# Kernel optimization log

Measured on AMD Instinct MI355X. Metric: run time of the kernel, lower is better.

The kernel has to match this reference:

```python
import jax, jax.numpy as jnp
import numpy as np

B, C, HD, H, W = 4, 64, 64, 64, 64  # batch, input_dim, hidden_dim, spatial


def conv1x1(x, w, b):
    # x: [B, Cin, H, W], w: [Cout, Cin], b: [Cout]
    return jnp.einsum('oc,bchw->bohw', w, x) + b[None, :, None, None]


def setup_inputs() -> dict:
    key = jax.random.key(0)
    ks = jax.random.split(key, 16)
    sc = lambda cin: 1.0 / np.sqrt(cin)
    d = {
        'h': jax.random.normal(ks[0], (B, C, H, W), jnp.float32),
        'm': jax.random.normal(ks[1], (B, C, H, W), jnp.float32),
        'Wq': jax.random.normal(ks[2], (HD, C), jnp.float32) * sc(C),
        'bq': jnp.zeros((HD,), jnp.float32),
        'Wk': jax.random.normal(ks[3], (HD, C), jnp.float32) * sc(C),
        'bk': jnp.zeros((HD,), jnp.float32),
        'Wk2': jax.random.normal(ks[4], (HD, C), jnp.float32) * sc(C),
        'bk2': jnp.zeros((HD,), jnp.float32),
        'Wv': jax.random.normal(ks[5], (C, C), jnp.float32) * sc(C),
        'bv': jnp.zeros((C,), jnp.float32),
        'Wv2': jax.random.normal(ks[6], (C, C), jnp.float32) * sc(C),
        'bv2': jnp.zeros((C,), jnp.float32),
        'Wz': jax.random.normal(ks[7], (2 * C, 2 * C), jnp.float32) * sc(2 * C),
        'bz': jnp.zeros((2 * C,), jnp.float32),
        'Wm': jax.random.normal(ks[8], (3 * C, 3 * C), jnp.float32) * sc(3 * C),
        'bm': jnp.zeros((3 * C,), jnp.float32),
    }
    return d


def reference(h, m, Wq, bq, Wk, bk, Wk2, bk2, Wv, bv, Wv2, bv2, Wz, bz, Wm, bm):
    b, c, hh, ww = h.shape
    n = hh * ww
    K_h = conv1x1(h, Wk, bk).reshape(b, HD, n)            # [B, HD, N]
    Q_h = conv1x1(h, Wq, bq).reshape(b, HD, n).transpose(0, 2, 1)  # [B, N, HD]
    V_h = conv1x1(h, Wv, bv).reshape(b, c, n)             # [B, C, N]
    K_m = conv1x1(m, Wk2, bk2).reshape(b, HD, n)
    V_m = conv1x1(m, Wv2, bv2).reshape(b, c, n)

    A_h = jax.nn.softmax(jnp.einsum('bnd,bdk->bnk', Q_h, K_h), axis=-1)  # [B, N, N]
    Z_h = jnp.einsum('bnk,bck->bcn', A_h, V_h).reshape(b, c, hh, ww)
    A_m = jax.nn.softmax(jnp.einsum('bnd,bdk->bnk', Q_h, K_m), axis=-1)
    Z_m = jnp.einsum('bnk,bck->bcn', A_m, V_m).reshape(b, c, hh, ww)

    Z = conv1x1(jnp.concatenate([Z_h, Z_m], axis=1), Wz, bz)   # [B, 2C, H, W]
    combined = conv1x1(jnp.concatenate([Z, h], axis=1), Wm, bm)  # [B, 3C, H, W]
    mo, mg, mi = jnp.split(combined, 3, axis=1)
    mi = jax.nn.sigmoid(mi)
    new_m = (1.0 - mi) * m + mi * jnp.tanh(mg)
    new_h = jax.nn.sigmoid(mo) * new_m
    return (new_h, new_m)
```

## Files before the change

kernel.cpp:

```cpp
#include <hip/hip_runtime.h>

#define BN 4
#define NN 4096
#define SPLITK 4
#define KTILE 64
#define LOG2E 1.44269504f
#define MFIX 36.0f

typedef __attribute__((ext_vector_type(8))) __bf16 bf16x8;
typedef __attribute__((ext_vector_type(8))) short s16x8;
typedef __attribute__((ext_vector_type(4))) float f32x4;
typedef unsigned short u16;

__device__ __forceinline__ u16 f2bf(float x) {
  unsigned int u = __builtin_bit_cast(unsigned int, x);
  u = (u + 0x7fffu + ((u >> 16) & 1u)) >> 16;
  return (u16)u;
}
__device__ __forceinline__ u16 f2bfs(float x) {
  __bf16 b = (__bf16)x;
  return __builtin_bit_cast(u16, b);
}

__device__ __forceinline__ float fexp2(float x) {
#if defined(__HIP_DEVICE_COMPILE__) && __has_builtin(__builtin_amdgcn_exp2f)
  return __builtin_amdgcn_exp2f(x);
#else
  return __builtin_exp2f(x);
#endif
}

__device__ __forceinline__ f32x4 mfma32(bf16x8 a, bf16x8 b, f32x4 c) {
#if defined(__HIP_DEVICE_COMPILE__)
  return __builtin_amdgcn_mfma_f32_16x16x32_bf16(a, b, c, 0, 0, 0);
#else
  (void)a; (void)b;
  return c;
#endif
}

__device__ __forceinline__ void gld16(const u16* g, u16* l) {
#if defined(__HIP_DEVICE_COMPILE__)
  __builtin_amdgcn_global_load_lds(
      (const __attribute__((address_space(1))) void*)g,
      (__attribute__((address_space(3))) void*)l, 16, 0, 0);
#else
  (void)g; (void)l;
#endif
}

#if defined(__HIP_DEVICE_COMPILE__)
#define SETPRIO(p) __builtin_amdgcn_s_setprio(p)
#else
#define SETPRIO(p)
#endif

#define PACK16(A, P0, P1)                                                          \
    P0.x = (unsigned)f2bf(A[0]) | ((unsigned)f2bf(A[1]) << 16);                    \
    P0.y = (unsigned)f2bf(A[2]) | ((unsigned)f2bf(A[3]) << 16);                    \
    P0.z = (unsigned)f2bf(A[4]) | ((unsigned)f2bf(A[5]) << 16);                    \
    P0.w = (unsigned)f2bf(A[6]) | ((unsigned)f2bf(A[7]) << 16);                    \
    P1.x = (unsigned)f2bf(A[8]) | ((unsigned)f2bf(A[9]) << 16);                    \
    P1.y = (unsigned)f2bf(A[10]) | ((unsigned)f2bf(A[11]) << 16);                  \
    P1.z = (unsigned)f2bf(A[12]) | ((unsigned)f2bf(A[13]) << 16);                  \
    P1.w = (unsigned)f2bf(A[14]) | ((unsigned)f2bf(A[15]) << 16);

__global__ __launch_bounds__(256) void fuse_w2_kernel(
    const float* __restrict__ Wz, const float* __restrict__ bz,
    const float* __restrict__ Wm, const float* __restrict__ bm,
    u16* __restrict__ Wbig, float* __restrict__ bbig) {
  __shared__ float wrow[128];
  __shared__ float bzs[128];
  int o = blockIdx.x;
  int t = threadIdx.x;
  if (t < 128) { wrow[t] = Wm[o * 192 + t]; bzs[t] = bz[t]; }
  __syncthreads();
  if (t < 128) {
    float s = 0.f;
#pragma unroll 4
    for (int j = 0; j < 128; ++j) s = fmaf(wrow[j], Wz[j * 128 + t], s);
    Wbig[o * 192 + t] = f2bf(s);
  } else if (t < 192) {
    Wbig[o * 192 + t] = f2bf(Wm[o * 192 + t]);
  } else if (t == 192) {
    float s = bm[o];
    for (int j = 0; j < 128; ++j) s = fmaf(wrow[j], bzs[j], s);
    bbig[o] = s;
  }
}

__global__ __launch_bounds__(256) void proj3_kernel(
    const float* __restrict__ h, const float* __restrict__ m,
    const float* __restrict__ Wq, const float* __restrict__ bq,
    const float* __restrict__ Wk, const float* __restrict__ bk,
    const float* __restrict__ Wk2, const float* __restrict__ bk2,
    const float* __restrict__ Wv, const float* __restrict__ bv,
    const float* __restrict__ Wv2, const float* __restrict__ bv2,
    u16* __restrict__ Q, u16* __restrict__ Kh, u16* __restrict__ Km,
    u16* __restrict__ Vh, u16* __restrict__ Vm, u16* __restrict__ hT) {
  __shared__ float xs[64][65];
  __shared__ float Wl[4096];
  int blk = blockIdx.x;
  int ntile = blk & 63, b = (blk >> 6) & 3, pid = blk >> 8;
  int n0 = ntile * 64;
  int t = threadIdx.x, nl = t & 63;
  const float* src = (pid == 2 || pid == 4) ? m : h;
  {
    int c0 = (t >> 6) * 16;
#pragma unroll
    for (int i = 0; i < 16; ++i) {
      int c = c0 + i;
      xs[c][nl] = src[((size_t)(b * 64) + c) * NN + n0 + nl];
    }
  }
  if (pid < 5) {
    const float* W = pid == 0 ? Wq : pid == 1 ? Wk : pid == 2 ? Wk2 : pid == 3 ? Wv : Wv2;
#pragma unroll
    for (int i = 0; i < 16; ++i) Wl[i * 256 + t] = W[i * 256 + t];
  }
  __syncthreads();
  int w = __builtin_amdgcn_readfirstlane(t >> 6);
  size_t nrow = (size_t)b * NN + n0 + nl;
  float acc[16];
  if (pid == 5) {
#pragma unroll
    for (int i = 0; i < 16; ++i) acc[i] = xs[w * 16 + i][nl];
  } else {
    const float* bs = pid == 0 ? bq : pid == 1 ? bk : pid == 2 ? bk2 : pid == 3 ? bv : bv2;
#pragma unroll
    for (int i = 0; i < 16; ++i) acc[i] = bs[w * 16 + i];
    for (int c = 0; c < 64; ++c) {
      float x = xs[c][nl];
#pragma unroll
      for (int i = 0; i < 16; ++i) acc[i] = fmaf(Wl[(w * 16 + i) * 64 + c], x, acc[i]);
    }
    if (pid == 0) {
#pragma unroll
      for (int i = 0; i < 16; ++i) acc[i] *= LOG2E;
    }
  }
  if (pid == 3 || pid == 4) {
    u16* dst = (pid == 3) ? Vh : Vm;
    int key = n0 + nl;
    size_t base = ((size_t)b << 18) + (size_t)(key >> 5) * 2048 + w * 512 +
                  (size_t)((key >> 3) & 3) * 128 + (key & 7);
#pragma unroll
    for (int i = 0; i < 16; ++i) dst[base + i * 8] = f2bf(acc[i]);
  } else {
    u16* dst = pid == 0 ? Q : pid == 1 ? Kh : pid == 2 ? Km : hT;
    uint4 p0, p1;
    PACK16(acc, p0, p1);
    uint4* dp = (uint4*)(dst + nrow * 64 + w * 16);
    dp[0] = p0; dp[1] = p1;
  }
}

__global__ __launch_bounds__(256, 4) void flash11_kernel(
    const u16* __restrict__ Qg, const u16* __restrict__ Khg,
    const u16* __restrict__ Kmg, const u16* __restrict__ Vhg,
    const u16* __restrict__ Vmg, u16* __restrict__ Opart,
    float* __restrict__ Lpart) {
  __shared__ u16 Kl[2][4096];
  __shared__ u16 Vl[2][4096];
  int blk = blockIdx.x;
  int combo = blk & 31, qt = blk >> 5;
  int attn = combo & 1, b = (combo >> 1) & 3, split = combo >> 3;
  const u16* K = (attn ? Kmg : Khg) + (size_t)b * NN * 64;
  const u16* V = (attn ? Vmg : Vhg) + ((size_t)b << 18);
  int t = threadIdx.x, wave = t >> 6, lane = t & 63, col = lane & 15, quad = lane >> 4;
  int row0 = qt * 128 + wave * 32;

  bf16x8 bq[2][2];
#pragma unroll
  for (int g = 0; g < 2; ++g) {
    const u16* qp = Qg + (size_t)b * NN * 64 + (size_t)(row0 + g * 16 + col) * 64 + quad * 8;
    bq[g][0] = *(const bf16x8*)(const void*)qp;
    bq[g][1] = *(const bf16x8*)(const void*)(qp + 32);
  }

  f32x4 O[2][4];
#pragma unroll
  for (int g = 0; g < 2; ++g)
#pragma unroll
    for (int i = 0; i < 4; ++i) O[g][i] = f32x4{0.f, 0.f, 0.f, 0.f};
  f32x4 Lacc[2];
  Lacc[0] = f32x4{0.f, 0.f, 0.f, 0.f};
  Lacc[1] = f32x4{0.f, 0.f, 0.f, 0.f};
  const f32x4 minit = {-MFIX, -MFIX, -MFIX, -MFIX};
  s16x8 onesv;
#pragma unroll
  for (int i = 0; i < 8; ++i) onesv[i] = (short)0x3F80;
  bf16x8 ones8 = __builtin_bit_cast(bf16x8, onesv);
  int sp = split * 8 + b * 2 + attn;

  const int kbase = split * (NN / SPLITK);
  const int TILES = NN / SPLITK / KTILE;

#define STAGE(BUF, K0)                                                           \
  _Pragma("unroll") for (int jj = 0; jj < 2; ++jj) {                             \
    int p = jj * 256 + t;                                                        \
    int krow_ = p >> 3;                                                          \
    int kj_ = (p & 7) ^ (krow_ & 7);                                             \
    int s5_ = krow_ & 31;                                                        \
    int tr_ = (krow_ & 32) | ((s5_ & 12) << 1) | (((s5_ >> 4) & 1) << 2) | (s5_ & 3); \
    gld16(K + (size_t)((K0) + tr_) * 64 + kj_ * 8, &Kl[BUF][p * 8]);             \
    gld16(V + (size_t)(K0) * 64 + p * 8, &Vl[BUF][p * 8]);                       \
  }

  STAGE(0, kbase);

  for (int kt = 0; kt < TILES; ++kt) {
    __syncthreads();
    int cur = kt & 1;
    if (kt + 1 < TILES) { STAGE(cur ^ 1, kbase + (kt + 1) * KTILE); }
    const u16* Kb = &Kl[cur][0];
    const u16* Vb = &Vl[cur][0];
    f32x4 St[4][2];
    SETPRIO(1);
#pragma unroll
    for (int nt = 0; nt < 4; ++nt) {
      int row = nt * 16 + col;
      int ph0 = row * 8 + (quad ^ (col & 7));
      int ph1 = row * 8 + ((4 + quad) ^ (col & 7));
      bf16x8 a0 = *(const bf16x8*)(const void*)(Kb + ph0 * 8);
      bf16x8 a1 = *(const bf16x8*)(const void*)(Kb + ph1 * 8);
#pragma unroll
      for (int g = 0; g < 2; ++g) {
        f32x4 acc = mfma32(a0, bq[g][0], minit);
        acc = mfma32(a1, bq[g][1], acc);
        St[nt][g] = acc;
      }
    }
    SETPRIO(0);
    bf16x8 pa[2][2];
#pragma unroll
    for (int grp = 0; grp < 2; ++grp)
#pragma unroll
      for (int g = 0; g < 2; ++g) {
        s16x8 pf;
#pragma unroll
        for (int r = 0; r < 4; ++r) {
          pf[r] = (short)f2bfs(fexp2(St[2 * grp][g][r]));
          pf[r + 4] = (short)f2bfs(fexp2(St[2 * grp + 1][g][r]));
        }
        bf16x8 p8 = __builtin_bit_cast(bf16x8, pf);
        pa[grp][g] = p8;
        Lacc[g] = mfma32(p8, ones8, Lacc[g]);
      }
    const u16* vbase = Vb + lane * 8;
    SETPRIO(1);
#pragma unroll
    for (int grp = 0; grp < 2; ++grp)
#pragma unroll
      for (int ct = 0; ct < 4; ++ct) {
        bf16x8 vf = *(const bf16x8*)(const void*)(vbase + grp * 2048 + ct * 512);
        O[0][ct] = mfma32(pa[grp][0], vf, O[0][ct]);
        O[1][ct] = mfma32(pa[grp][1], vf, O[1][ct]);
      }
    SETPRIO(0);
  }
#undef STAGE

#pragma unroll
  for (int g = 0; g < 2; ++g) {
#pragma unroll
    for (int ct = 0; ct < 4; ++ct)
#pragma unroll
      for (int r = 0; r < 4; ++r) {
        size_t q = (size_t)row0 + g * 16 + quad * 4 + r;
        Opart[((size_t)sp * NN + q) * 64 + ct * 16 + col] = f2bfs(O[g][ct][r]);
      }
    if (col == 0) {
#pragma unroll
      for (int r = 0; r < 4; ++r)
        Lpart[(size_t)sp * NN + row0 + g * 16 + quad * 4 + r] = Lacc[g][r];
    }
  }
}

__global__ __launch_bounds__(256) void epi3_kernel(
    const u16* __restrict__ Wb, const float* __restrict__ bb,
    const u16* __restrict__ Opart, const float* __restrict__ Lpart,
    const u16* __restrict__ hT, const float* __restrict__ mglob,
    float* __restrict__ out) {
  int blk = blockIdx.x;
  int ng = blk * 16;
  int b = ng >> 12;
  int t = threadIdx.x, wave = t >> 6, lane = t & 63, col = lane & 15, quad = lane >> 4;
  int qb = (ng & (NN - 1)) + col;
  float Lh = 0.f, Lm = 0.f;
#pragma unroll
  for (int s = 0; s < SPLITK; ++s) {
    Lh += Lpart[(size_t)(s * 8 + b * 2) * NN + qb];
    Lm += Lpart[(size_t)(s * 8 + b * 2 + 1) * NN + qb];
  }
  float invLh = 1.f / Lh;
  float invLm = 1.f / Lm;
  size_t nrow = ((size_t)ng + col) * 64;
  bf16x8 bfr[6];
#define MERGEF(DST, ATTN, OFF, INVL)                                             \
  {                                                                              \
    float s8_[8] = {0.f, 0.f, 0.f, 0.f, 0.f, 0.f, 0.f, 0.f};                     \
    _Pragma("unroll") for (int sp_ = 0; sp_ < SPLITK; ++sp_) {                   \
      const u16* p_ =                                                            \
          Opart + ((size_t)(sp_ * 8 + b * 2 + (ATTN)) * NN + qb) * 64 + (OFF);   \
      bf16x8 a_ = *(const bf16x8*)(const void*)p_;                               \
      _Pragma("unroll") for (int i = 0; i < 8; ++i) s8_[i] += (float)a_[i];      \
    }                                                                            \
    bf16x8 r_;                                                                   \
    _Pragma("unroll") for (int i = 0; i < 8; ++i)                                \
      r_[i] = (__bf16)(s8_[i] * (INVL));                                         \
    DST = r_;                                                                    \
  }
  MERGEF(bfr[0], 0, quad * 8, invLh);
  MERGEF(bfr[1], 0, 32 + quad * 8, invLh);
  MERGEF(bfr[2], 1, quad * 8, invLm);
  MERGEF(bfr[3], 1, 32 + quad * 8, invLm);
#undef MERGEF
  bfr[4] = *(const bf16x8*)(const void*)(hT + nrow + quad * 8);
  bfr[5] = *(const bf16x8*)(const void*)(hT + nrow + 32 + quad * 8);
  f32x4 acc[3];
#pragma unroll
  for (int j = 0; j < 3; ++j) {
    int mt = wave + j * 4;
#pragma unroll
    for (int r = 0; r < 4; ++r) acc[j][r] = bb[mt * 16 + quad * 4 + r];
  }
#pragma unroll
  for (int ks = 0; ks < 6; ++ks) {
#pragma unroll
    for (int j = 0; j < 3; ++j) {
      int mt = wave + j * 4;
      bf16x8 af = *(const bf16x8*)(const void*)(Wb + (size_t)(mt * 16 + col) * 192 + ks * 32 + quad * 8);
      acc[j] = mfma32(af, bfr[ks], acc[j]);
    }
  }
  int nloc = (ng & (NN - 1)) + col;
#pragma unroll
  for (int r = 0; r < 4; ++r) {
    int o = wave * 16 + quad * 4 + r;
    float mo = acc[0][r], mgt = acc[1][r], mi = acc[2][r];
    float si = 1.f / (1.f + fexp2(-mi * LOG2E));
    float tg = 1.f - 2.f / (fexp2(2.f * LOG2E * mgt) + 1.f);
    float mv = mglob[(size_t)(b * 64 + o) * NN + nloc];
    float nm = (1.f - si) * mv + si * tg;
    float nh = nm / (1.f + fexp2(-mo * LOG2E));
    out[(size_t)(b * 64 + o) * NN + nloc] = nh;
    out[(size_t)BN * 64 * NN + (size_t)(b * 64 + o) * NN + nloc] = nm;
  }
}

extern "C" void kernel_launch(void* const* d_in, const int* in_sizes, int n_in,
                              void* d_out, int out_size, void* d_ws, size_t ws_size,
                              hipStream_t stream) {
  const float* h = (const float*)d_in[0];
  const float* m = (const float*)d_in[1];
  const float* Wq = (const float*)d_in[2];
  const float* bq = (const float*)d_in[3];
  const float* Wk = (const float*)d_in[4];
  const float* bk = (const float*)d_in[5];
  const float* Wk2 = (const float*)d_in[6];
  const float* bk2 = (const float*)d_in[7];
  const float* Wv = (const float*)d_in[8];
  const float* bv = (const float*)d_in[9];
  const float* Wv2 = (const float*)d_in[10];
  const float* bv2 = (const float*)d_in[11];
  const float* Wz = (const float*)d_in[12];
  const float* bz = (const float*)d_in[13];
  const float* Wm = (const float*)d_in[14];
  const float* bm = (const float*)d_in[15];
  float* out = (float*)d_out;

  size_t off = 0;
  auto alloc = [&](size_t bytes) {
    void* p = (char*)d_ws + off;
    off += (bytes + 255) & ~(size_t)255;
    return p;
  };
  const size_t bn64 = (size_t)BN * NN * 64;
  u16* Q  = (u16*)alloc(bn64 * 2);
  u16* Kh = (u16*)alloc(bn64 * 2);
  u16* Km = (u16*)alloc(bn64 * 2);
  u16* Vh = (u16*)alloc(bn64 * 2);
  u16* Vm = (u16*)alloc(bn64 * 2);
  u16* hT = (u16*)alloc(bn64 * 2);
  u16* Opart = (u16*)alloc((size_t)SPLITK * 8 * NN * 64 * 2);
  float* Lpart = (float*)alloc((size_t)SPLITK * 8 * NN * 4);
  u16* Wbigbf = (u16*)alloc(192 * 192 * 2);
  float* bbig = (float*)alloc(192 * 4);
  (void)ws_size; (void)in_sizes; (void)n_in; (void)out_size;

  fuse_w2_kernel<<<192, 256, 0, stream>>>(Wz, bz, Wm, bm, Wbigbf, bbig);
  proj3_kernel<<<6 * BN * 64, 256, 0, stream>>>(h, m, Wq, bq, Wk, bk, Wk2, bk2, Wv, bv,
                                                Wv2, bv2, Q, Kh, Km, Vh, Vm, hT);
  flash11_kernel<<<32 * 32, 256, 0, stream>>>(Q, Kh, Km, Vh, Vm, Opart, Lpart);
  epi3_kernel<<<(BN * NN) / 16, 256, 0, stream>>>(Wbigbf, bbig, Opart, Lpart, hT, m, out);
}
```

Measured before the change: 168.6 us.

## Compute input projections with split-bf16 MFMA and share input tiles across projections

```diff
diff --git a/kernel.cpp b/kernel.cpp
--- a/kernel.cpp
+++ b/kernel.cpp
@@ -20,6 +20,10 @@
 __device__ __forceinline__ u16 f2bfs(float x) {
   __bf16 b = (__bf16)x;
   return __builtin_bit_cast(u16, b);
+}
+__device__ __forceinline__ float bf2f(u16 s) {
+  unsigned int u = ((unsigned int)s) << 16;
+  return __builtin_bit_cast(float, u);
 }
 
 __device__ __forceinline__ float fexp2(float x) {
@@ -55,24 +59,31 @@
 #define SETPRIO(p)
 #endif
 
-#define PACK16(A, P0, P1)                                                          \
-    P0.x = (unsigned)f2bf(A[0]) | ((unsigned)f2bf(A[1]) << 16);                    \
-    P0.y = (unsigned)f2bf(A[2]) | ((unsigned)f2bf(A[3]) << 16);                    \
-    P0.z = (unsigned)f2bf(A[4]) | ((unsigned)f2bf(A[5]) << 16);                    \
-    P0.w = (unsigned)f2bf(A[6]) | ((unsigned)f2bf(A[7]) << 16);                    \
-    P1.x = (unsigned)f2bf(A[8]) | ((unsigned)f2bf(A[9]) << 16);                    \
-    P1.y = (unsigned)f2bf(A[10]) | ((unsigned)f2bf(A[11]) << 16);                  \
-    P1.z = (unsigned)f2bf(A[12]) | ((unsigned)f2bf(A[13]) << 16);                  \
-    P1.w = (unsigned)f2bf(A[14]) | ((unsigned)f2bf(A[15]) << 16);
-
 __global__ __launch_bounds__(256) void fuse_w2_kernel(
     const float* __restrict__ Wz, const float* __restrict__ bz,
     const float* __restrict__ Wm, const float* __restrict__ bm,
-    u16* __restrict__ Wbig, float* __restrict__ bbig) {
+    const float* __restrict__ Wq, const float* __restrict__ Wk,
+    const float* __restrict__ Wk2, const float* __restrict__ Wv,
+    const float* __restrict__ Wv2,
+    u16* __restrict__ Wbig, float* __restrict__ bbig, u16* __restrict__ Wall) {
   __shared__ float wrow[128];
   __shared__ float bzs[128];
+  int t = threadIdx.x;
+  if (blockIdx.x >= 192) {
+    int pid = blockIdx.x - 192;
+    const float* Wsrc = pid == 0 ? Wq : pid == 1 ? Wk : pid == 2 ? Wk2 : pid == 3 ? Wv : Wv2;
+    float sc = (pid == 0) ? LOG2E : 1.f;
+#pragma unroll
+    for (int i = 0; i < 16; ++i) {
+      int idx = t * 16 + i;
+      float w = Wsrc[idx] * sc;
+      u16 hu = f2bf(w);
+      Wall[pid * 4096 + idx] = hu;
+      Wall[5 * 4096 + pid * 4096 + idx] = f2bf(w - bf2f(hu));
+    }
+    return;
+  }
   int o = blockIdx.x;
-  int t = threadIdx.x;
   if (t < 128) { wrow[t] = Wm[o * 192 + t]; bzs[t] = bz[t]; }
   __syncthreads();
   if (t < 128) {
@@ -89,69 +100,93 @@
   }
 }
 
-__global__ __launch_bounds__(256) void proj3_kernel(
+__global__ __launch_bounds__(256) void proj7_kernel(
+    const u16* __restrict__ Wall,
+    const float* __restrict__ bq, const float* __restrict__ bk,
+    const float* __restrict__ bk2, const float* __restrict__ bv,
+    const float* __restrict__ bv2,
     const float* __restrict__ h, const float* __restrict__ m,
-    const float* __restrict__ Wq, const float* __restrict__ bq,
-    const float* __restrict__ Wk, const float* __restrict__ bk,
-    const float* __restrict__ Wk2, const float* __restrict__ bk2,
-    const float* __restrict__ Wv, const float* __restrict__ bv,
-    const float* __restrict__ Wv2, const float* __restrict__ bv2,
     u16* __restrict__ Q, u16* __restrict__ Kh, u16* __restrict__ Km,
     u16* __restrict__ Vh, u16* __restrict__ Vm, u16* __restrict__ hT) {
   __shared__ float xs[64][65];
-  __shared__ float Wl[4096];
   int blk = blockIdx.x;
-  int ntile = blk & 63, b = (blk >> 6) & 3, pid = blk >> 8;
-  int n0 = ntile * 64;
-  int t = threadIdx.x, nl = t & 63;
-  const float* src = (pid == 2 || pid == 4) ? m : h;
+  int nt = blk & 63, b = (blk >> 6) & 3, src_m = blk >> 8;
+  const float* src = src_m ? m : h;
+  int t = threadIdx.x, lane = t & 63, w = t >> 6, col = lane & 15, quad = lane >> 4;
+  int n0 = nt * 64;
   {
-    int c0 = (t >> 6) * 16;
-#pragma unroll
-    for (int i = 0; i < 16; ++i) {
-      int c = c0 + i;
-      xs[c][nl] = src[((size_t)(b * 64) + c) * NN + n0 + nl];
-    }
-  }
-  if (pid < 5) {
-    const float* W = pid == 0 ? Wq : pid == 1 ? Wk : pid == 2 ? Wk2 : pid == 3 ? Wv : Wv2;
-#pragma unroll
-    for (int i = 0; i < 16; ++i) Wl[i * 256 + t] = W[i * 256 + t];
+    int c0 = w * 16, nl = lane;
+#pragma unroll
+    for (int i = 0; i < 16; ++i)
+      xs[c0 + i][nl] = src[((size_t)(b * 64) + c0 + i) * NN + n0 + nl];
   }
   __syncthreads();
-  int w = __builtin_amdgcn_readfirstlane(t >> 6);
-  size_t nrow = (size_t)b * NN + n0 + nl;
-  float acc[16];
-  if (pid == 5) {
-#pragma unroll
-    for (int i = 0; i < 16; ++i) acc[i] = xs[w * 16 + i][nl];
+  int nloc = w * 16 + col;
+  bf16x8 xh[2], xl[2];
+#pragma unroll
+  for (int half = 0; half < 2; ++half) {
+    bf16x8 hh, ll;
+#pragma unroll
+    for (int j = 0; j < 8; ++j) {
+      float x = xs[half * 32 + quad * 8 + j][nloc];
+      u16 hu = f2bf(x);
+      hh[j] = __builtin_bit_cast(__bf16, hu);
+      ll[j] = (__bf16)(x - bf2f(hu));
+    }
+    xh[half] = hh; xl[half] = ll;
+  }
+  if (!src_m) {
+    int cj = lane & 7, nr = lane >> 3;
+#pragma unroll
+    for (int it = 0; it < 2; ++it) {
+      int n = w * 16 + it * 8 + nr;
+      bf16x8 hi8;
+#pragma unroll
+      for (int i = 0; i < 8; ++i)
+        hi8[i] = __builtin_bit_cast(__bf16, f2bf(xs[cj * 8 + i][n]));
+      *(bf16x8*)(void*)(hT + ((size_t)b * NN + n0 + n) * 64 + cj * 8) = hi8;
+    }
+  }
+  int glob_n = n0 + nloc;
+  auto do_proj = [&](int pid, const float* bias, u16* dstQK, u16* dstV) {
+    const u16* Whi = Wall + pid * 4096;
+    const u16* Wlo = Wall + 5 * 4096 + pid * 4096;
+    float sc = (pid == 0) ? LOG2E : 1.f;
+#pragma unroll
+    for (int ot = 0; ot < 4; ++ot) {
+      size_t wb = (size_t)(ot * 16 + col) * 64 + quad * 8;
+      bf16x8 wh0 = *(const bf16x8*)(const void*)(Whi + wb);
+      bf16x8 wh1 = *(const bf16x8*)(const void*)(Whi + wb + 32);
+      bf16x8 wl0 = *(const bf16x8*)(const void*)(Wlo + wb);
+      bf16x8 wl1 = *(const bf16x8*)(const void*)(Wlo + wb + 32);
+      float4 b4 = *(const float4*)(bias + ot * 16 + quad * 4);
+      f32x4 c = {b4.x * sc, b4.y * sc, b4.z * sc, b4.w * sc};
+      c = mfma32(wh0, xh[0], c);
+      c = mfma32(wh1, xh[1], c);
+      c = mfma32(wh0, xl[0], c);
+      c = mfma32(wh1, xl[1], c);
+      c = mfma32(wl0, xh[0], c);
+      c = mfma32(wl1, xh[1], c);
+      if (dstQK) {
+        uint2 p;
+        p.x = (unsigned)f2bf(c[0]) | ((unsigned)f2bf(c[1]) << 16);
+        p.y = (unsigned)f2bf(c[2]) | ((unsigned)f2bf(c[3]) << 16);
+        *(uint2*)(void*)(dstQK + ((size_t)b * NN + glob_n) * 64 + ot * 16 + quad * 4) = p;
+      } else {
+        size_t base = ((size_t)b << 18) + (size_t)(glob_n >> 5) * 2048 + ot * 512 +
+                      (size_t)((glob_n >> 3) & 3) * 128 + (glob_n & 7);
+#pragma unroll
+        for (int r = 0; r < 4; ++r) dstV[base + (quad * 4 + r) * 8] = f2bf(c[r]);
+      }
+    }
+  };
+  if (!src_m) {
+    do_proj(0, bq, Q, nullptr);
+    do_proj(1, bk, Kh, nullptr);
+    do_proj(3, bv, nullptr, Vh);
   } else {
-    const float* bs = pid == 0 ? bq : pid == 1 ? bk : pid == 2 ? bk2 : pid == 3 ? bv : bv2;
-#pragma unroll
-    for (int i = 0; i < 16; ++i) acc[i] = bs[w * 16 + i];
-    for (int c = 0; c < 64; ++c) {
-      float x = xs[c][nl];
-#pragma unroll
-      for (int i = 0; i < 16; ++i) acc[i] = fmaf(Wl[(w * 16 + i) * 64 + c], x, acc[i]);
-    }
-    if (pid == 0) {
-#pragma unroll
-      for (int i = 0; i < 16; ++i) acc[i] *= LOG2E;
-    }
-  }
-  if (pid == 3 || pid == 4) {
-    u16* dst = (pid == 3) ? Vh : Vm;
-    int key = n0 + nl;
-    size_t base = ((size_t)b << 18) + (size_t)(key >> 5) * 2048 + w * 512 +
-                  (size_t)((key >> 3) & 3) * 128 + (key & 7);
-#pragma unroll
-    for (int i = 0; i < 16; ++i) dst[base + i * 8] = f2bf(acc[i]);
-  } else {
-    u16* dst = pid == 0 ? Q : pid == 1 ? Kh : pid == 2 ? Km : hT;
-    uint4 p0, p1;
-    PACK16(acc, p0, p1);
-    uint4* dp = (uint4*)(dst + nrow * 64 + w * 16);
-    dp[0] = p0; dp[1] = p1;
+    do_proj(2, bk2, Km, nullptr);
+    do_proj(4, bv2, nullptr, Vm);
   }
 }
 
@@ -388,11 +423,13 @@
   float* Lpart = (float*)alloc((size_t)SPLITK * 8 * NN * 4);
   u16* Wbigbf = (u16*)alloc(192 * 192 * 2);
   float* bbig = (float*)alloc(192 * 4);
+  u16* Wall = (u16*)alloc((size_t)2 * 5 * 4096 * 2);
   (void)ws_size; (void)in_sizes; (void)n_in; (void)out_size;
 
-  fuse_w2_kernel<<<192, 256, 0, stream>>>(Wz, bz, Wm, bm, Wbigbf, bbig);
-  proj3_kernel<<<6 * BN * 64, 256, 0, stream>>>(h, m, Wq, bq, Wk, bk, Wk2, bk2, Wv, bv,
-                                                Wv2, bv2, Q, Kh, Km, Vh, Vm, hT);
+  fuse_w2_kernel<<<197, 256, 0, stream>>>(Wz, bz, Wm, bm, Wq, Wk, Wk2, Wv, Wv2,
+                                          Wbigbf, bbig, Wall);
+  proj7_kernel<<<2 * BN * 64, 256, 0, stream>>>(Wall, bq, bk, bk2, bv, bv2, h, m,
+                                                Q, Kh, Km, Vh, Vm, hT);
   flash11_kernel<<<32 * 32, 256, 0, stream>>>(Q, Kh, Km, Vh, Vm, Opart, Lpart);
   epi3_kernel<<<(BN * NN) / 16, 256, 0, stream>>>(Wbigbf, bbig, Opart, Lpart, hT, m, out);
 }
```

Measured after the change: 167.7 us. Within noise of the previous version (-0.5%).
